# Optimization experiments

Measured on AMD Instinct MI355X. Metric: run time of the kernel, lower is better.

Reference implementation:

```python
import jax, jax.numpy as jnp
import numpy as np

ANCHORS = np.array([[10.0, 13.0], [16.0, 30.0], [33.0, 23.0]], dtype=np.float32)
NUM_ANCHORS = 3
NUM_CLASSES = 80
OBJ_SCALE = 1.0
NOOBJ_SCALE = 100.0
EPS = 1e-12


def setup_inputs() -> dict:
    key = jax.random.key(0)
    ks = jax.random.split(key, 10)
    B, A, G, C = 32, NUM_ANCHORS, 52, NUM_CLASSES
    x = jax.random.normal(ks[0], (B, A * (C + 5), G, G), dtype=jnp.float32)
    tx = jax.random.uniform(ks[1], (B, A, G, G), dtype=jnp.float32)
    ty = jax.random.uniform(ks[2], (B, A, G, G), dtype=jnp.float32)
    tw = jax.random.normal(ks[3], (B, A, G, G), dtype=jnp.float32)
    th = jax.random.normal(ks[4], (B, A, G, G), dtype=jnp.float32)
    tconf = jax.random.uniform(ks[5], (B, A, G, G), dtype=jnp.float32)
    tcls = jax.random.uniform(ks[6], (B, A, G, G, C), dtype=jnp.float32)
    sum_weights1 = jax.random.uniform(ks[7], (B, A, G, G), dtype=jnp.float32)
    obj_mask = jax.random.randint(ks[8], (B, A, G, G), 0, 2).astype(bool)
    noobj_mask = jax.random.randint(ks[9], (B, A, G, G), 0, 2).astype(bool)
    return {"x": x, "tx": tx, "ty": ty, "tw": tw, "th": th, "tconf": tconf,
            "tcls": tcls, "sum_weights1": sum_weights1, "obj_mask": obj_mask,
            "noobj_mask": noobj_mask, "img_dim": 416}


def _bce(p, t):
    # torch BCELoss(reduction='none') on already-sigmoided probs
    return -(t * jnp.log(jnp.clip(p, EPS, 1.0)) + (1.0 - t) * jnp.log(jnp.clip(1.0 - p, EPS, 1.0)))


def reference(x, tx, ty, tw, th, tconf, tcls, sum_weights1, obj_mask, noobj_mask, img_dim):
    B, _, G, _ = x.shape
    A, C = NUM_ANCHORS, NUM_CLASSES
    stride = img_dim / G  # python float
    # [B, A, G, G, C+5]
    pred = x.reshape(B, A, C + 5, G, G).transpose(0, 1, 3, 4, 2)
    px = jax.nn.sigmoid(pred[..., 0])
    py = jax.nn.sigmoid(pred[..., 1])
    pw = pred[..., 2]
    ph = pred[..., 3]
    pred_conf = jax.nn.sigmoid(pred[..., 4])
    pred_cls = jax.nn.sigmoid(pred[..., 5:])

    grid_x = jnp.arange(G, dtype=x.dtype).reshape(1, 1, 1, G)  # varies along last axis
    grid_y = jnp.arange(G, dtype=x.dtype).reshape(1, 1, G, 1)
    scaled_anchors = jnp.asarray(ANCHORS) / jnp.asarray(stride, x.dtype)
    anchor_w = scaled_anchors[:, 0].reshape(1, A, 1, 1)
    anchor_h = scaled_anchors[:, 1].reshape(1, A, 1, 1)

    sg = jax.lax.stop_gradient  # mimics .data in pred_boxes construction
    pred_boxes = jnp.stack([
        sg(px) + jnp.broadcast_to(grid_x, px.shape),
        sg(py) + jnp.broadcast_to(grid_y, py.shape),
        jnp.exp(sg(pw)) * jnp.broadcast_to(anchor_w, pw.shape),
        jnp.exp(sg(ph)) * jnp.broadcast_to(anchor_h, ph.shape),
    ], axis=-1)  # [B, A, G, G, 4]

    output = jnp.concatenate([
        pred_boxes.reshape(B, -1, 4) * stride,
        pred_conf.reshape(B, -1, 1),
        pred_cls.reshape(B, -1, C),
    ], axis=-1)

    om = obj_mask.astype(x.dtype)
    nm = noobj_mask.astype(x.dtype)
    n_obj = jnp.maximum(om.sum(), 1.0)
    n_noobj = jnp.maximum(nm.sum(), 1.0)

    def wmse(p, t):
        # mean over obj elements of mse * sum_weights1
        return jnp.sum(om * (p - t) ** 2 * sum_weights1) / n_obj

    loss_x = wmse(px, tx)
    loss_y = wmse(py, ty)
    loss_w = wmse(pw, tw)
    loss_h = wmse(ph, th)

    bce_conf = _bce(pred_conf, tconf)
    loss_conf_obj = jnp.sum(om * bce_conf * sum_weights1) / n_obj
    loss_conf_noobj = jnp.sum(nm * bce_conf) / n_noobj
    loss_conf = OBJ_SCALE * loss_conf_obj + NOOBJ_SCALE * loss_conf_noobj

    # tcls[obj_mask] yields [N, C]; mean is over N*C
    loss_cls = jnp.sum(om[..., None] * _bce(pred_cls, tcls)) / (n_obj * C)

    total_loss = loss_x + loss_y + loss_w + loss_h + loss_conf + loss_cls
    return output, total_loss
```

## Files before the change

kernel.cpp:

```cpp
#include <hip/hip_runtime.h>

#define NB 32
#define NA 3
#define GD 52
#define GG 2704
#define NC 80
#define CHN 85
#define CPW 8
#define WPP 338
#define NPLANE (NB * NA)
#define NWAVE (NPLANE * WPP)
#define WPB 4
#define NBLK (NWAVE / WPB)
#define NXQ 170
#define NTQ 160
#define LXW 680
#define AUXW 72
#define RBLK 32
#define NEG_LN2_80 (-0.008664339757f)

__device__ __forceinline__ float sigm_u(float u) { return __builtin_amdgcn_rcpf(u); }

__global__ __launch_bounds__(256) void yolo_main(
    const float* __restrict__ x,
    const float* __restrict__ tx, const float* __restrict__ ty,
    const float* __restrict__ tw, const float* __restrict__ th,
    const float* __restrict__ tconf, const float* __restrict__ tcls,
    const float* __restrict__ sw1,
    const int* __restrict__ om, const int* __restrict__ nm,
    const int* __restrict__ imgdim,
    float* __restrict__ out,
    float4* __restrict__ partials,
    double* __restrict__ accD)
{
    __shared__ float lx_all[WPB * LXW];
    __shared__ float la_all[WPB * AUXW];

    const int tid  = threadIdx.x;
    const int widx = tid >> 6, lane = tid & 63;
    const int wid  = blockIdx.x * WPB + widx;
    const int plane = wid / WPP;
    const int sblk  = wid - plane * WPP;
    const int a = plane % NA, b = plane / NA;
    const int s0 = sblk * CPW;
    float* lx = lx_all + widx * LXW;
    float* la = la_all + widx * AUXW;

    int iv = imgdim[0];
    float imgf = (iv > 0 && iv < 65536) ? (float)iv : __int_as_float(iv);
    const float stride = imgf / (float)GD;
    const float aw = (a == 0) ? 10.0f : ((a == 1) ? 16.0f : 33.0f);
    const float ah = (a == 0) ? 13.0f : ((a == 1) ? 30.0f : 23.0f);

    const long pbase = (long)plane * GG + s0;
    const float* xb = x + ((long)b * (NA * CHN) + a * CHN) * GG + s0;
    const float* tb = tcls + pbase * NC;

    float4 xr[3];
    #pragma unroll
    for (int k = 0; k < 3; ++k) {
        int q = lane + 64 * k;
        if (q < NXQ) {
            int ch = q >> 1, sq = (q & 1) << 2;
            xr[k] = *(const float4*)(xb + (long)ch * GG + sq);
        }
    }

    const int sc = lane & 7;
    float r_tx = tx[pbase + sc], r_ty = ty[pbase + sc];
    float r_tw = tw[pbase + sc], r_th = th[pbase + sc];
    float r_tc = tconf[pbase + sc], r_sw = sw1[pbase + sc];
    float r_om = (float)om[pbase + sc], r_nm = (float)nm[pbase + sc];

    float4 tr[3]; float gk[3];
    #pragma unroll
    for (int k = 0; k < 3; ++k) {
        gk[k] = 0.0f;
        int q = lane + 64 * k;
        if (q < NTQ) {
            int s = q / 20, c4 = (q - s * 20) * 4;
            float g = __shfl(r_om, s, 8);
            gk[k] = g;
            if (g != 0.0f) tr[k] = *(const float4*)(tb + s * NC + c4);
        }
    }

    if (lane < CPW) {
        int gcell = s0 + lane;
        int gyi = gcell / GD;
        la[0 * CPW + lane] = r_tx;  la[1 * CPW + lane] = r_ty;
        la[2 * CPW + lane] = r_tw;  la[3 * CPW + lane] = r_th;
        la[4 * CPW + lane] = r_tc;  la[5 * CPW + lane] = r_om * r_sw;
        la[6 * CPW + lane] = r_nm;
        la[7 * CPW + lane] = (float)(gcell - gyi * GD);
        la[8 * CPW + lane] = (float)gyi;
    }
    __builtin_amdgcn_wave_barrier();

    float s_obj = 0.f, s_cn = 0.f, s_cl2 = 0.f;

    #pragma unroll
    for (int k = 0; k < 3; ++k) {
        int q = lane + 64 * k;
        if (q >= NXQ) continue;
        int ch = q >> 1, sq = (q & 1) << 2;
        float vv[4] = { xr[k].x, xr[k].y, xr[k].z, xr[k].w };
        if (ch >= 5) {
            #pragma unroll
            for (int j = 0; j < 4; ++j)
                lx[(sq + j) * CHN + ch] = sigm_u(1.0f + __expf(-vv[j]));
        } else if (ch == 0) {
            #pragma unroll
            for (int j = 0; j < 4; ++j) {
                int s = sq + j;
                float p = sigm_u(1.0f + __expf(-vv[j]));
                float d = p - la[0 * CPW + s];
                s_obj = fmaf(la[5 * CPW + s], d * d, s_obj);
                lx[s * CHN + 0] = (p + la[7 * CPW + s]) * stride;
            }
        } else if (ch == 1) {
            #pragma unroll
            for (int j = 0; j < 4; ++j) {
                int s = sq + j;
                float p = sigm_u(1.0f + __expf(-vv[j]));
                float d = p - la[1 * CPW + s];
                s_obj = fmaf(la[5 * CPW + s], d * d, s_obj);
                lx[s * CHN + 1] = (p + la[8 * CPW + s]) * stride;
            }
        } else if (ch == 2) {
            #pragma unroll
            for (int j = 0; j < 4; ++j) {
                int s = sq + j;
                float d = vv[j] - la[2 * CPW + s];
                s_obj = fmaf(la[5 * CPW + s], d * d, s_obj);
                lx[s * CHN + 2] = __expf(vv[j]) * aw;
            }
        } else if (ch == 3) {
            #pragma unroll
            for (int j = 0; j < 4; ++j) {
                int s = sq + j;
                float d = vv[j] - la[3 * CPW + s];
                s_obj = fmaf(la[5 * CPW + s], d * d, s_obj);
                lx[s * CHN + 3] = __expf(vv[j]) * ah;
            }
        } else {
            #pragma unroll
            for (int j = 0; j < 4; ++j) {
                int s = sq + j;
                float z = vv[j];
                float u = 1.0f + __expf(-z);
                float p = sigm_u(u);
                float t = la[4 * CPW + s];
                float bb = fmaf(1.0f - t, z, __logf(u));
                s_obj = fmaf(la[5 * CPW + s], bb, s_obj);
                s_cn  = fmaf(la[6 * CPW + s], bb, s_cn);
                lx[s * CHN + 4] = p;
            }
        }
    }
    __builtin_amdgcn_wave_barrier();

    float* ob = out + pbase * CHN;
    #pragma unroll
    for (int k = 0; k < 3; ++k) {
        int q = lane + 64 * k;
        if (q < NXQ) {
            float4 w4 = *(const float4*)&lx[4 * q];
            *(float4*)(ob + 4 * q) = w4;
        }
    }

    #pragma unroll
    for (int k = 0; k < 3; ++k) {
        if (gk[k] != 0.0f) {
            int q = lane + 64 * k;
            int s = q / 20, c4 = (q - s * 20) * 4;
            int base = s * CHN + 5 + c4;
            float tt[4] = { tr[k].x, tr[k].y, tr[k].z, tr[k].w };
            #pragma unroll
            for (int j = 0; j < 4; ++j) {
                float p  = lx[base + j];
                float l0 = __log2f(p);
                float l1 = __log2f(1.0f - p);
                s_cl2 += fmaf(tt[j], l0 - l1, l1);
            }
        }
    }
    s_obj = fmaf(s_cl2, NEG_LN2_80, s_obj);

    float v0 = (lane < CPW) ? r_om : 0.0f;
    float v1 = (lane < CPW) ? r_nm : 0.0f;
    float v2 = s_obj, v3 = s_cn;
    #pragma unroll
    for (int off = 32; off > 0; off >>= 1) {
        v0 += __shfl_down(v0, off, 64);
        v1 += __shfl_down(v1, off, 64);
        v2 += __shfl_down(v2, off, 64);
        v3 += __shfl_down(v3, off, 64);
    }
    if (lane == 0) {
        if (partials) {
            partials[wid] = make_float4(v0, v1, v2, v3);
        } else {
            atomicAdd(&accD[0], (double)v0);
            atomicAdd(&accD[8], (double)v1);
            atomicAdd(&accD[16], (double)v2);
            atomicAdd(&accD[24], (double)v3);
        }
    }
}

__global__ __launch_bounds__(256) void yolo_reduceA(const float4* __restrict__ partials,
                                                    float4* __restrict__ stage2)
{
    __shared__ float sred[4][4];
    const int tid = threadIdx.x, wv = tid >> 6, ln = tid & 63;
    float d0 = 0, d1 = 0, d2 = 0, d3 = 0;
    for (int i = blockIdx.x * 256 + tid; i < NWAVE; i += RBLK * 256) {
        float4 p = partials[i];
        d0 += p.x; d1 += p.y; d2 += p.z; d3 += p.w;
    }
    #pragma unroll
    for (int off = 32; off > 0; off >>= 1) {
        d0 += __shfl_down(d0, off, 64);
        d1 += __shfl_down(d1, off, 64);
        d2 += __shfl_down(d2, off, 64);
        d3 += __shfl_down(d3, off, 64);
    }
    if (ln == 0) { sred[wv][0] = d0; sred[wv][1] = d1; sred[wv][2] = d2; sred[wv][3] = d3; }
    __syncthreads();
    if (tid == 0)
        stage2[blockIdx.x] = make_float4(sred[0][0] + sred[1][0] + sred[2][0] + sred[3][0],
                                         sred[0][1] + sred[1][1] + sred[2][1] + sred[3][1],
                                         sred[0][2] + sred[1][2] + sred[2][2] + sred[3][2],
                                         sred[0][3] + sred[1][3] + sred[2][3] + sred[3][3]);
}

__global__ __launch_bounds__(64) void yolo_reduceB(const float4* __restrict__ stage2,
                                                   float* __restrict__ out_loss)
{
    const int ln = threadIdx.x;
    double d0 = 0, d1 = 0, d2 = 0, d3 = 0;
    if (ln < RBLK) {
        float4 p = stage2[ln];
        d0 = p.x; d1 = p.y; d2 = p.z; d3 = p.w;
    }
    #pragma unroll
    for (int off = 32; off > 0; off >>= 1) {
        d0 += __shfl_down(d0, off, 64);
        d1 += __shfl_down(d1, off, 64);
        d2 += __shfl_down(d2, off, 64);
        d3 += __shfl_down(d3, off, 64);
    }
    if (ln == 0) {
        double nobj = fmax(d0, 1.0), nnoobj = fmax(d1, 1.0);
        *out_loss = (float)(d2 / nobj + 100.0 * d3 / nnoobj);
    }
}

__global__ void yolo_final_atomic(const double* __restrict__ accD, float* __restrict__ out_loss)
{
    double nobj = fmax(accD[0], 1.0), nnoobj = fmax(accD[8], 1.0);
    *out_loss = (float)(accD[16] / nobj + 100.0 * accD[24] / nnoobj);
}

extern "C" void kernel_launch(void* const* d_in, const int* in_sizes, int n_in,
                              void* d_out, int out_size, void* d_ws, size_t ws_size,
                              hipStream_t stream)
{
    const float* x     = (const float*)d_in[0];
    const float* tx    = (const float*)d_in[1];
    const float* ty    = (const float*)d_in[2];
    const float* tw    = (const float*)d_in[3];
    const float* th    = (const float*)d_in[4];
    const float* tconf = (const float*)d_in[5];
    const float* tcls  = (const float*)d_in[6];
    const float* sw1   = (const float*)d_in[7];
    const int*   om    = (const int*)d_in[8];
    const int*   nm    = (const int*)d_in[9];
    const int*   img   = (const int*)d_in[10];
    float* out = (float*)d_out;

    const size_t need = (size_t)(NWAVE + RBLK) * sizeof(float4);
    dim3 grid(NBLK);

    if (ws_size >= need) {
        float4* partials = (float4*)d_ws;
        float4* stage2   = partials + NWAVE;
        yolo_main<<<grid, 256, 0, stream>>>(x, tx, ty, tw, th, tconf, tcls, sw1,
                                            om, nm, img, out, partials, nullptr);
        yolo_reduceA<<<RBLK, 256, 0, stream>>>(partials, stage2);
        yolo_reduceB<<<1, 64, 0, stream>>>(stage2, out + (out_size - 1));
    } else {
        double* accD = (double*)d_ws;
        hipMemsetAsync(d_ws, 0, 32 * sizeof(double), stream);
        yolo_main<<<grid, 256, 0, stream>>>(x, tx, ty, tw, th, tconf, tcls, sw1,
                                            om, nm, img, out, nullptr, accD);
        yolo_final_atomic<<<1, 1, 0, stream>>>(accD, out + (out_size - 1));
    }
}
```

Before: 54.73 us.

## Process 16 cells per wave in two 8-cell halves with upfront x loads

Each wave now covers 16 grid cells instead of 8, halving the wave count. It loads both halves of the x tile up front, then runs transform, store and class BCE for each half in turn, reusing the same LDS staging buffer. The goal is more memory-level parallelism per wave and less per-wave fixed overhead such as the aux loads, setup and reduction. In exchange, register pressure rises from holding six float4s, and the tcls loads are now issued after the x loads, which may expose their latency.

```diff
diff --git a/kernel.cpp b/kernel.cpp
--- a/kernel.cpp
+++ b/kernel.cpp
@@ -6,16 +6,17 @@
 #define GG 2704
 #define NC 80
 #define CHN 85
-#define CPW 8
-#define WPP 338
+#define CPW 16
+#define CSW 8
+#define WPP 169
 #define NPLANE (NB * NA)
 #define NWAVE (NPLANE * WPP)
 #define WPB 4
 #define NBLK (NWAVE / WPB)
-#define NXQ 170
-#define NTQ 160
+#define NXQ8 170
+#define NTQ8 160
 #define LXW 680
-#define AUXW 72
+#define AUXW 144
 #define RBLK 32
 #define NEG_LN2_80 (-0.008664339757f)
 
@@ -56,34 +57,22 @@
     const float* xb = x + ((long)b * (NA * CHN) + a * CHN) * GG + s0;
     const float* tb = tcls + pbase * NC;
 
-    float4 xr[3];
+    float4 xrA[3], xrB[3];
     #pragma unroll
     for (int k = 0; k < 3; ++k) {
-        int q = lane + 64 * k;
-        if (q < NXQ) {
-            int ch = q >> 1, sq = (q & 1) << 2;
-            xr[k] = *(const float4*)(xb + (long)ch * GG + sq);
+        int p = lane + 64 * k;
+        if (p < NXQ8) {
+            int ch = p >> 1, sq = (p & 1) << 2;
+            xrA[k] = *(const float4*)(xb + (long)ch * GG + sq);
+            xrB[k] = *(const float4*)(xb + (long)ch * GG + CSW + sq);
         }
     }
 
-    const int sc = lane & 7;
+    const int sc = lane & 15;
     float r_tx = tx[pbase + sc], r_ty = ty[pbase + sc];
     float r_tw = tw[pbase + sc], r_th = th[pbase + sc];
     float r_tc = tconf[pbase + sc], r_sw = sw1[pbase + sc];
     float r_om = (float)om[pbase + sc], r_nm = (float)nm[pbase + sc];
-
-    float4 tr[3]; float gk[3];
-    #pragma unroll
-    for (int k = 0; k < 3; ++k) {
-        gk[k] = 0.0f;
-        int q = lane + 64 * k;
-        if (q < NTQ) {
-            int s = q / 20, c4 = (q - s * 20) * 4;
-            float g = __shfl(r_om, s, 8);
-            gk[k] = g;
-            if (g != 0.0f) tr[k] = *(const float4*)(tb + s * NC + c4);
-        }
-    }
 
     if (lane < CPW) {
         int gcell = s0 + lane;
@@ -98,94 +87,127 @@
     __builtin_amdgcn_wave_barrier();
 
     float s_obj = 0.f, s_cn = 0.f, s_cl2 = 0.f;
-
-    #pragma unroll
-    for (int k = 0; k < 3; ++k) {
-        int q = lane + 64 * k;
-        if (q >= NXQ) continue;
-        int ch = q >> 1, sq = (q & 1) << 2;
-        float vv[4] = { xr[k].x, xr[k].y, xr[k].z, xr[k].w };
-        if (ch >= 5) {
-            #pragma unroll
-            for (int j = 0; j < 4; ++j)
-                lx[(sq + j) * CHN + ch] = sigm_u(1.0f + __expf(-vv[j]));
-        } else if (ch == 0) {
-            #pragma unroll
-            for (int j = 0; j < 4; ++j) {
-                int s = sq + j;
-                float p = sigm_u(1.0f + __expf(-vv[j]));
-                float d = p - la[0 * CPW + s];
-                s_obj = fmaf(la[5 * CPW + s], d * d, s_obj);
-                lx[s * CHN + 0] = (p + la[7 * CPW + s]) * stride;
-            }
-        } else if (ch == 1) {
-            #pragma unroll
-            for (int j = 0; j < 4; ++j) {
-                int s = sq + j;
-                float p = sigm_u(1.0f + __expf(-vv[j]));
-                float d = p - la[1 * CPW + s];
-                s_obj = fmaf(la[5 * CPW + s], d * d, s_obj);
-                lx[s * CHN + 1] = (p + la[8 * CPW + s]) * stride;
-            }
-        } else if (ch == 2) {
-            #pragma unroll
-            for (int j = 0; j < 4; ++j) {
-                int s = sq + j;
-                float d = vv[j] - la[2 * CPW + s];
-                s_obj = fmaf(la[5 * CPW + s], d * d, s_obj);
-                lx[s * CHN + 2] = __expf(vv[j]) * aw;
-            }
-        } else if (ch == 3) {
-            #pragma unroll
-            for (int j = 0; j < 4; ++j) {
-                int s = sq + j;
-                float d = vv[j] - la[3 * CPW + s];
-                s_obj = fmaf(la[5 * CPW + s], d * d, s_obj);
-                lx[s * CHN + 3] = __expf(vv[j]) * ah;
-            }
-        } else {
-            #pragma unroll
-            for (int j = 0; j < 4; ++j) {
-                int s = sq + j;
-                float z = vv[j];
-                float u = 1.0f + __expf(-z);
-                float p = sigm_u(u);
-                float t = la[4 * CPW + s];
-                float bb = fmaf(1.0f - t, z, __logf(u));
-                s_obj = fmaf(la[5 * CPW + s], bb, s_obj);
-                s_cn  = fmaf(la[6 * CPW + s], bb, s_cn);
-                lx[s * CHN + 4] = p;
-            }
-        }
-    }
+    float4 tr[3]; float gk[3];
+
+#define TCLS_ISSUE(P)                                                          \
+    _Pragma("unroll")                                                          \
+    for (int k = 0; k < 3; ++k) {                                              \
+        gk[k] = 0.0f;                                                          \
+        int q = lane + 64 * k;                                                 \
+        if (q < NTQ8) {                                                        \
+            int s = q / 20, c4 = (q - s * 20) * 4;                             \
+            float g = __shfl(r_om, (P) * CSW + s, 16);                         \
+            gk[k] = g;                                                         \
+            if (g != 0.0f)                                                     \
+                tr[k] = *(const float4*)(tb + ((P) * CSW + s) * NC + c4);      \
+        }                                                                      \
+    }
+
+#define TRANSFORM(P, XR)                                                       \
+    _Pragma("unroll")                                                          \
+    for (int k = 0; k < 3; ++k) {                                              \
+        int q = lane + 64 * k;                                                 \
+        if (q >= NXQ8) continue;                                               \
+        int ch = q >> 1, sq = (q & 1) << 2;                                    \
+        float vv[4] = { XR[k].x, XR[k].y, XR[k].z, XR[k].w };                  \
+        if (ch >= 5) {                                                         \
+            _Pragma("unroll")                                                  \
+            for (int j = 0; j < 4; ++j)                                        \
+                lx[(sq + j) * CHN + ch] = sigm_u(1.0f + __expf(-vv[j]));       \
+        } else if (ch == 0) {                                                  \
+            _Pragma("unroll")                                                  \
+            for (int j = 0; j < 4; ++j) {                                      \
+                int s = sq + j, sa = (P) * CSW + s;                            \
+                float p = sigm_u(1.0f + __expf(-vv[j]));                       \
+                float d = p - la[0 * CPW + sa];                                \
+                s_obj = fmaf(la[5 * CPW + sa], d * d, s_obj);                  \
+                lx[s * CHN + 0] = (p + la[7 * CPW + sa]) * stride;             \
+            }                                                                  \
+        } else if (ch == 1) {                                                  \
+            _Pragma("unroll")                                                  \
+            for (int j = 0; j < 4; ++j) {                                      \
+                int s = sq + j, sa = (P) * CSW + s;                            \
+                float p = sigm_u(1.0f + __expf(-vv[j]));                       \
+                float d = p - la[1 * CPW + sa];                                \
+                s_obj = fmaf(la[5 * CPW + sa], d * d, s_obj);                  \
+                lx[s * CHN + 1] = (p + la[8 * CPW + sa]) * stride;             \
+            }                                                                  \
+        } else if (ch == 2) {                                                  \
+            _Pragma("unroll")                                                  \
+            for (int j = 0; j < 4; ++j) {                                      \
+                int s = sq + j, sa = (P) * CSW + s;                            \
+                float d = vv[j] - la[2 * CPW + sa];                            \
+                s_obj = fmaf(la[5 * CPW + sa], d * d, s_obj);                  \
+                lx[s * CHN + 2] = __expf(vv[j]) * aw;                          \
+            }                                                                  \
+        } else if (ch == 3) {                                                  \
+            _Pragma("unroll")                                                  \
+            for (int j = 0; j < 4; ++j) {                                      \
+                int s = sq + j, sa = (P) * CSW + s;                            \
+                float d = vv[j] - la[3 * CPW + sa];                            \
+                s_obj = fmaf(la[5 * CPW + sa], d * d, s_obj);                  \
+                lx[s * CHN + 3] = __expf(vv[j]) * ah;                          \
+            }                                                                  \
+        } else {                                                               \
+            _Pragma("unroll")                                                  \
+            for (int j = 0; j < 4; ++j) {                                      \
+                int s = sq + j, sa = (P) * CSW + s;                            \
+                float z = vv[j];                                               \
+                float u = 1.0f + __expf(-z);                                   \
+                float p = sigm_u(u);                                           \
+                float t = la[4 * CPW + sa];                                    \
+                float bb = fmaf(1.0f - t, z, __logf(u));                       \
+                s_obj = fmaf(la[5 * CPW + sa], bb, s_obj);                     \
+                s_cn  = fmaf(la[6 * CPW + sa], bb, s_cn);                      \
+                lx[s * CHN + 4] = p;                                           \
+            }                                                                  \
+        }                                                                      \
+    }
+
+#define STORE_OUT(P)                                                           \
+    {                                                                          \
+        float* ob = out + (pbase + (P) * CSW) * CHN;                           \
+        _Pragma("unroll")                                                      \
+        for (int k = 0; k < 3; ++k) {                                          \
+            int q = lane + 64 * k;                                             \
+            if (q < NXQ8) {                                                    \
+                float4 w4 = *(const float4*)&lx[4 * q];                        \
+                *(float4*)(ob + 4 * q) = w4;                                   \
+            }                                                                  \
+        }                                                                      \
+    }
+
+#define CLS_BCE()                                                              \
+    _Pragma("unroll")                                                          \
+    for (int k = 0; k < 3; ++k) {                                              \
+        if (gk[k] != 0.0f) {                                                   \
+            int q = lane + 64 * k;                                             \
+            int s = q / 20, c4 = (q - s * 20) * 4;                             \
+            int base = s * CHN + 5 + c4;                                       \
+            float tt[4] = { tr[k].x, tr[k].y, tr[k].z, tr[k].w };              \
+            _Pragma("unroll")                                                  \
+            for (int j = 0; j < 4; ++j) {                                      \
+                float p  = lx[base + j];                                       \
+                float l0 = __log2f(p);                                         \
+                float l1 = __log2f(1.0f - p);                                  \
+                s_cl2 += fmaf(tt[j], l0 - l1, l1);                             \
+            }                                                                  \
+        }                                                                      \
+    }
+
+    TCLS_ISSUE(0)
+    TRANSFORM(0, xrA)
     __builtin_amdgcn_wave_barrier();
-
-    float* ob = out + pbase * CHN;
-    #pragma unroll
-    for (int k = 0; k < 3; ++k) {
-        int q = lane + 64 * k;
-        if (q < NXQ) {
-            float4 w4 = *(const float4*)&lx[4 * q];
-            *(float4*)(ob + 4 * q) = w4;
-        }
-    }
-
-    #pragma unroll
-    for (int k = 0; k < 3; ++k) {
-        if (gk[k] != 0.0f) {
-            int q = lane + 64 * k;
-            int s = q / 20, c4 = (q - s * 20) * 4;
-            int base = s * CHN + 5 + c4;
-            float tt[4] = { tr[k].x, tr[k].y, tr[k].z, tr[k].w };
-            #pragma unroll
-            for (int j = 0; j < 4; ++j) {
-                float p  = lx[base + j];
-                float l0 = __log2f(p);
-                float l1 = __log2f(1.0f - p);
-                s_cl2 += fmaf(tt[j], l0 - l1, l1);
-            }
-        }
-    }
+    STORE_OUT(0)
+    CLS_BCE()
+    __builtin_amdgcn_wave_barrier();
+
+    TCLS_ISSUE(1)
+    TRANSFORM(1, xrB)
+    __builtin_amdgcn_wave_barrier();
+    STORE_OUT(1)
+    CLS_BCE()
+
     s_obj = fmaf(s_cl2, NEG_LN2_80, s_obj);
 
     float v0 = (lane < CPW) ? r_om : 0.0f;
```

After: 53.97 us. No clear change (-1.4%).

## Fuse class BCE into sigmoid pass using logits and double cells per wave

Applied to the files above, without the earlier changes.

Each wave now handles 16 cells instead of 8, and blocks shrink to 2 waves. The class BCE is computed from the logits inside the transform loop as (1-t)*z + log(1+e^-z), in log2 units. This removes the second pass that reread LDS and took two logs per element. tcls is now read as scalar loads laid out to match the x channel mapping and prefetched in a ping-pong order alongside the transforms. In exchange, tcls loads become scalar strided gathers rather than float4, and each wave holds more registers.

```diff
diff --git a/kernel.cpp b/kernel.cpp
--- a/kernel.cpp
+++ b/kernel.cpp
@@ -6,22 +6,22 @@
 #define GG 2704
 #define NC 80
 #define CHN 85
-#define CPW 8
-#define WPP 338
+#define CPW 16
+#define WPP 169
 #define NPLANE (NB * NA)
 #define NWAVE (NPLANE * WPP)
-#define WPB 4
+#define WPB 2
 #define NBLK (NWAVE / WPB)
-#define NXQ 170
-#define NTQ 160
-#define LXW 680
-#define AUXW 72
+#define NXQ 340
+#define LXW 1360
+#define AUXW 160
 #define RBLK 32
-#define NEG_LN2_80 (-0.008664339757f)
+#define LN2_80 (0.008664339757f)
+#define INV_LN2 (1.4426950408889634f)
 
 __device__ __forceinline__ float sigm_u(float u) { return __builtin_amdgcn_rcpf(u); }
 
-__global__ __launch_bounds__(256) void yolo_main(
+__global__ __launch_bounds__(128) void yolo_main(
     const float* __restrict__ x,
     const float* __restrict__ tx, const float* __restrict__ ty,
     const float* __restrict__ tw, const float* __restrict__ th,
@@ -56,34 +56,21 @@
     const float* xb = x + ((long)b * (NA * CHN) + a * CHN) * GG + s0;
     const float* tb = tcls + pbase * NC;
 
-    float4 xr[3];
-    #pragma unroll
-    for (int k = 0; k < 3; ++k) {
+    float4 xr[6];
+    #pragma unroll
+    for (int k = 0; k < 6; ++k) {
         int q = lane + 64 * k;
         if (q < NXQ) {
-            int ch = q >> 1, sq = (q & 1) << 2;
+            int ch = q >> 2, sq = (q & 3) << 2;
             xr[k] = *(const float4*)(xb + (long)ch * GG + sq);
         }
     }
 
-    const int sc = lane & 7;
+    const int sc = lane & 15;
     float r_tx = tx[pbase + sc], r_ty = ty[pbase + sc];
     float r_tw = tw[pbase + sc], r_th = th[pbase + sc];
     float r_tc = tconf[pbase + sc], r_sw = sw1[pbase + sc];
     float r_om = (float)om[pbase + sc], r_nm = (float)nm[pbase + sc];
-
-    float4 tr[3]; float gk[3];
-    #pragma unroll
-    for (int k = 0; k < 3; ++k) {
-        gk[k] = 0.0f;
-        int q = lane + 64 * k;
-        if (q < NTQ) {
-            int s = q / 20, c4 = (q - s * 20) * 4;
-            float g = __shfl(r_om, s, 8);
-            gk[k] = g;
-            if (g != 0.0f) tr[k] = *(const float4*)(tb + s * NC + c4);
-        }
-    }
 
     if (lane < CPW) {
         int gcell = s0 + lane;
@@ -94,75 +81,111 @@
         la[6 * CPW + lane] = r_nm;
         la[7 * CPW + lane] = (float)(gcell - gyi * GD);
         la[8 * CPW + lane] = (float)gyi;
+        la[9 * CPW + lane] = r_om;
     }
     __builtin_amdgcn_wave_barrier();
 
     float s_obj = 0.f, s_cn = 0.f, s_cl2 = 0.f;
-
-    #pragma unroll
-    for (int k = 0; k < 3; ++k) {
-        int q = lane + 64 * k;
-        if (q >= NXQ) continue;
-        int ch = q >> 1, sq = (q & 1) << 2;
-        float vv[4] = { xr[k].x, xr[k].y, xr[k].z, xr[k].w };
-        if (ch >= 5) {
-            #pragma unroll
-            for (int j = 0; j < 4; ++j)
-                lx[(sq + j) * CHN + ch] = sigm_u(1.0f + __expf(-vv[j]));
-        } else if (ch == 0) {
-            #pragma unroll
-            for (int j = 0; j < 4; ++j) {
-                int s = sq + j;
-                float p = sigm_u(1.0f + __expf(-vv[j]));
-                float d = p - la[0 * CPW + s];
-                s_obj = fmaf(la[5 * CPW + s], d * d, s_obj);
-                lx[s * CHN + 0] = (p + la[7 * CPW + s]) * stride;
-            }
-        } else if (ch == 1) {
-            #pragma unroll
-            for (int j = 0; j < 4; ++j) {
-                int s = sq + j;
-                float p = sigm_u(1.0f + __expf(-vv[j]));
-                float d = p - la[1 * CPW + s];
-                s_obj = fmaf(la[5 * CPW + s], d * d, s_obj);
-                lx[s * CHN + 1] = (p + la[8 * CPW + s]) * stride;
-            }
-        } else if (ch == 2) {
-            #pragma unroll
-            for (int j = 0; j < 4; ++j) {
-                int s = sq + j;
-                float d = vv[j] - la[2 * CPW + s];
-                s_obj = fmaf(la[5 * CPW + s], d * d, s_obj);
-                lx[s * CHN + 2] = __expf(vv[j]) * aw;
-            }
-        } else if (ch == 3) {
-            #pragma unroll
-            for (int j = 0; j < 4; ++j) {
-                int s = sq + j;
-                float d = vv[j] - la[3 * CPW + s];
-                s_obj = fmaf(la[5 * CPW + s], d * d, s_obj);
-                lx[s * CHN + 3] = __expf(vv[j]) * ah;
-            }
-        } else {
-            #pragma unroll
-            for (int j = 0; j < 4; ++j) {
-                int s = sq + j;
-                float z = vv[j];
-                float u = 1.0f + __expf(-z);
-                float p = sigm_u(u);
-                float t = la[4 * CPW + s];
-                float bb = fmaf(1.0f - t, z, __logf(u));
-                s_obj = fmaf(la[5 * CPW + s], bb, s_obj);
-                s_cn  = fmaf(la[6 * CPW + s], bb, s_cn);
-                lx[s * CHN + 4] = p;
-            }
-        }
-    }
+    float tA[4], tB[4];
+
+#define TPREF(K, T)                                                            \
+    {                                                                          \
+        int q = lane + 64 * (K);                                               \
+        int ch = q >> 2, sq = (q & 3) << 2;                                    \
+        _Pragma("unroll")                                                      \
+        for (int j = 0; j < 4; ++j) {                                          \
+            T[j] = 0.0f;                                                       \
+            int s = sq + j;                                                    \
+            if (q < NXQ && ch >= 5 && la[9 * CPW + s] != 0.0f)                 \
+                T[j] = tb[s * NC + (ch - 5)];                                  \
+        }                                                                      \
+    }
+
+#define XFORM(K, T)                                                            \
+    {                                                                          \
+        int q = lane + 64 * (K);                                               \
+        if (q < NXQ) {                                                         \
+            int ch = q >> 2, sq = (q & 3) << 2;                                \
+            float vv[4] = { xr[K].x, xr[K].y, xr[K].z, xr[K].w };              \
+            if (ch >= 5) {                                                     \
+                _Pragma("unroll")                                              \
+                for (int j = 0; j < 4; ++j) {                                  \
+                    int s = sq + j;                                            \
+                    float z = vv[j];                                           \
+                    float u = 1.0f + __expf(-z);                               \
+                    lx[s * CHN + ch] = sigm_u(u);                              \
+                    float o = la[9 * CPW + s];                                 \
+                    float e = fmaf(1.0f - T[j], z * INV_LN2, __log2f(u));      \
+                    s_cl2 = fmaf(o, e, s_cl2);                                 \
+                }                                                              \
+            } else if (ch == 0) {                                              \
+                _Pragma("unroll")                                              \
+                for (int j = 0; j < 4; ++j) {                                  \
+                    int s = sq + j;                                            \
+                    float p = sigm_u(1.0f + __expf(-vv[j]));                   \
+                    float d = p - la[0 * CPW + s];                             \
+                    s_obj = fmaf(la[5 * CPW + s], d * d, s_obj);               \
+                    lx[s * CHN + 0] = (p + la[7 * CPW + s]) * stride;          \
+                }                                                              \
+            } else if (ch == 1) {                                              \
+                _Pragma("unroll")                                              \
+                for (int j = 0; j < 4; ++j) {                                  \
+                    int s = sq + j;                                            \
+                    float p = sigm_u(1.0f + __expf(-vv[j]));                   \
+                    float d = p - la[1 * CPW + s];                             \
+                    s_obj = fmaf(la[5 * CPW + s], d * d, s_obj);               \
+                    lx[s * CHN + 1] = (p + la[8 * CPW + s]) * stride;          \
+                }                                                              \
+            } else if (ch == 2) {                                              \
+                _Pragma("unroll")                                              \
+                for (int j = 0; j < 4; ++j) {                                  \
+                    int s = sq + j;                                            \
+                    float d = vv[j] - la[2 * CPW + s];                         \
+                    s_obj = fmaf(la[5 * CPW + s], d * d, s_obj);               \
+                    lx[s * CHN + 2] = __expf(vv[j]) * aw;                      \
+                }                                                              \
+            } else if (ch == 3) {                                              \
+                _Pragma("unroll")                                              \
+                for (int j = 0; j < 4; ++j) {                                  \
+                    int s = sq + j;                                            \
+                    float d = vv[j] - la[3 * CPW + s];                         \
+                    s_obj = fmaf(la[5 * CPW + s], d * d, s_obj);               \
+                    lx[s * CHN + 3] = __expf(vv[j]) * ah;                      \
+                }                                                              \
+            } else {                        \
+                _Pragma("unroll")                                              \
+                for (int j = 0; j < 4; ++j) {                                  \
+                    int s = sq + j;                                            \
+                    float z = vv[j];                                           \
+                    float u = 1.0f + __expf(-z);                               \
+                    float p = sigm_u(u);                                       \
+                    float t = la[4 * CPW + s];                                 \
+                    float bb = fmaf(1.0f - t, z, __logf(u));                   \
+                    s_obj = fmaf(la[5 * CPW + s], bb, s_obj);                  \
+                    s_cn  = fmaf(la[6 * CPW + s], bb, s_cn);                   \
+                    lx[s * CHN + 4] = p;                                       \
+                }                                                              \
+            }                                                                  \
+        }                                                                      \
+    }
+
+    TPREF(0, tA)
+    TPREF(1, tB)
+    XFORM(0, tA)
+    TPREF(2, tA)
+    XFORM(1, tB)
+    TPREF(3, tB)
+    XFORM(2, tA)
+    TPREF(4, tA)
+    XFORM(3, tB)
+    TPREF(5, tB)
+    XFORM(4, tA)
+    XFORM(5, tB)
     __builtin_amdgcn_wave_barrier();
 
     float* ob = out + pbase * CHN;
     #pragma unroll
-    for (int k = 0; k < 3; ++k) {
+    for (int k = 0; k < 6; ++k) {
         int q = lane + 64 * k;
         if (q < NXQ) {
             float4 w4 = *(const float4*)&lx[4 * q];
@@ -170,23 +193,7 @@
         }
     }
 
-    #pragma unroll
-    for (int k = 0; k < 3; ++k) {
-        if (gk[k] != 0.0f) {
-            int q = lane + 64 * k;
-            int s = q / 20, c4 = (q - s * 20) * 4;
-            int base = s * CHN + 5 + c4;
-            float tt[4] = { tr[k].x, tr[k].y, tr[k].z, tr[k].w };
-            #pragma unroll
-            for (int j = 0; j < 4; ++j) {
-                float p  = lx[base + j];
-                float l0 = __log2f(p);
-                float l1 = __log2f(1.0f - p);
-                s_cl2 += fmaf(tt[j], l0 - l1, l1);
-            }
-        }
-    }
-    s_obj = fmaf(s_cl2, NEG_LN2_80, s_obj);
+    s_obj = fmaf(s_cl2, LN2_80, s_obj);
 
     float v0 = (lane < CPW) ? r_om : 0.0f;
     float v1 = (lane < CPW) ? r_nm : 0.0f;
@@ -287,14 +294,14 @@
     if (ws_size >= need) {
         float4* partials = (float4*)d_ws;
         float4* stage2   = partials + NWAVE;
-        yolo_main<<<grid, 256, 0, stream>>>(x, tx, ty, tw, th, tconf, tcls, sw1,
+        yolo_main<<<grid, 128, 0, stream>>>(x, tx, ty, tw, th, tconf, tcls, sw1,
                                             om, nm, img, out, partials, nullptr);
         yolo_reduceA<<<RBLK, 256, 0, stream>>>(partials, stage2);
         yolo_reduceB<<<1, 64, 0, stream>>>(stage2, out + (out_size - 1));
     } else {
         double* accD = (double*)d_ws;
         hipMemsetAsync(d_ws, 0, 32 * sizeof(double), stream);
-        yolo_main<<<grid, 256, 0, stream>>>(x, tx, ty, tw, th, tconf, tcls, sw1,
+        yolo_main<<<grid, 128, 0, stream>>>(x, tx, ty, tw, th, tconf, tcls, sw1,
                                             om, nm, img, out, nullptr, accD);
         yolo_final_atomic<<<1, 1, 0, stream>>>(accD, out + (out_size - 1));
     }
```

Result: no change. 54.22 us (median of 2 runs) (-0.9%).
